# Optimization experiments

Hardware: AMD Instinct MI355X
Metric: run time of the kernel (lower is better)

The kernel has to match this reference:

```python
import jax, jax.numpy as jnp
import numpy as np

N = 50000      # clusters (nodes)
E = 800000     # edges
C_IN = 128     # pt_tr_in_channels
C_OUT = 128    # pt_tr_out_channels
P_HID = 64     # pos_nn hidden
A_HID = 64     # attn_nn hidden
DIM = 2        # pt_tr_dim


def setup_inputs() -> dict:
    key = jax.random.key(0)
    ks = jax.random.split(key, 12)
    def w(k, i, o):
        return jax.random.normal(k, (i, o), jnp.float32) / np.float32(np.sqrt(i))
    return {
        "x": jax.random.normal(ks[0], (N, C_IN), jnp.float32),
        "pos": jax.random.uniform(ks[1], (N, DIM), jnp.float32),
        "edge_index": jax.random.randint(ks[2], (2, E), 0, N),
        # PointTransformerConv linear projections (bias=False in PyG)
        "W_lin": w(ks[3], C_IN, C_OUT),
        "W_src": w(ks[4], C_IN, C_OUT),
        "W_dst": w(ks[5], C_IN, C_OUT),
        # pos_nn MLP [DIM, P_HID, C_OUT], plain_last=False -> ReLU after both layers
        "Wp1": w(ks[6], DIM, P_HID), "bp1": jnp.zeros((P_HID,), jnp.float32),
        "Wp2": w(ks[7], P_HID, C_OUT), "bp2": jnp.zeros((C_OUT,), jnp.float32),
        # attn_nn MLP [C_OUT, A_HID, C_OUT]
        "Wa1": w(ks[8], C_OUT, A_HID), "ba1": jnp.zeros((A_HID,), jnp.float32),
        "Wa2": w(ks[9], A_HID, C_OUT), "ba2": jnp.zeros((C_OUT,), jnp.float32),
    }


def _mlp2(x, W1, b1, W2, b2):
    # PyG MLP(plain_last=False) at eval: Linear -> (identity BN) -> ReLU, twice
    return jax.nn.relu(jax.nn.relu(x @ W1 + b1) @ W2 + b2)


def _segment_softmax(logits, seg, num_segments):
    # per-destination, per-channel stable softmax over incoming edges
    m = jax.ops.segment_max(logits, seg, num_segments=num_segments)  # [N, C]
    e = jnp.exp(logits - m[seg])
    s = jax.ops.segment_sum(e, seg, num_segments=num_segments)
    return e / (s[seg] + 1e-16)


def reference(x, pos, edge_index, W_lin, W_src, W_dst,
              Wp1, bp1, Wp2, bp2, Wa1, ba1, Wa2, ba2):
    src, dst = edge_index[0], edge_index[1]          # message j -> i
    h = x @ W_lin                                     # value path  [N, C]
    a_src = (x @ W_src)[src]                          # alpha_j     [E, C]
    a_dst = (x @ W_dst)[dst]                          # alpha_i     [E, C]
    delta = _mlp2(pos[dst] - pos[src], Wp1, bp1, Wp2, bp2)   # [E, C]
    alpha = _mlp2(a_dst - a_src + delta, Wa1, ba1, Wa2, ba2) # [E, C]
    alpha = _segment_softmax(alpha, dst, N)
    out = jax.ops.segment_sum(alpha * (h[src] + delta), dst, num_segments=N)
    return jax.nn.relu(out)  # out['clusters'].relu()
```

## Files before the change

### kernel.cpp

```cpp
#include <hip/hip_runtime.h>
#include <hip/hip_bf16.h>

#define NN 50000
#define NE 800000

typedef short s16x8 __attribute__((ext_vector_type(8)));
typedef float f32x4 __attribute__((ext_vector_type(4)));

__device__ __forceinline__ unsigned packbf2(float a, float b) {
  __hip_bfloat162 h = __float22bfloat162_rn(make_float2(a, b));
  return *reinterpret_cast<unsigned*>(&h);
}
__device__ __forceinline__ unsigned short bf16rn(float x) {
  return (unsigned short)(packbf2(x, x) & 0xffffu);
}

__global__ __launch_bounds__(256) void zero_counts(int* __restrict__ counts) {
  const int i = blockIdx.x * 256 + threadIdx.x;
  if (i < NN) counts[i] = 0;
}

__global__ __launch_bounds__(256) void count_kernel(const int* __restrict__ ei,
                                                    int* __restrict__ counts) {
  const int e = blockIdx.x * 256 + threadIdx.x;
  if (e < NE) atomicAdd(&counts[ei[NE + e]], 1);
}

__global__ __launch_bounds__(256) void scan_block(const int* __restrict__ counts,
                                                  int* __restrict__ ep,
                                                  int* __restrict__ blocksum) {
  const int i = blockIdx.x * 256 + threadIdx.x;
  const int lane = threadIdx.x & 63;
  const int w = threadIdx.x >> 6;
  const int v = (i < NN) ? counts[i] : 0;
  int s = v;
  #pragma unroll
  for (int off = 1; off < 64; off <<= 1) {
    const int t = __shfl_up(s, off, 64);
    if (lane >= off) s += t;
  }
  __shared__ int wsums[4];
  if (lane == 63) wsums[w] = s;
  __syncthreads();
  int add = 0;
  for (int j = 0; j < w; ++j) add += wsums[j];
  s += add;
  if (i < NN) ep[i] = s - v;
  if (threadIdx.x == 255) blocksum[blockIdx.x] = s;
}

__global__ void scan_tops(const int* __restrict__ blocksum,
                          int* __restrict__ blockoff, int n) {
  const int lane = threadIdx.x;
  int carry = 0;
  for (int base = 0; base < n; base += 64) {
    const int i = base + lane;
    const int v = (i < n) ? blocksum[i] : 0;
    int s = v;
    #pragma unroll
    for (int off = 1; off < 64; off <<= 1) {
      const int t = __shfl_up(s, off, 64);
      if (lane >= off) s += t;
    }
    s += carry;
    if (i < n) blockoff[i] = s - v;
    carry = __shfl(s, 63, 64);
  }
}

__global__ __launch_bounds__(256) void scan_finish(const int* __restrict__ ep,
                                                   const int* __restrict__ blockoff,
                                                   int* __restrict__ cursor,
                                                   int* __restrict__ rowptr) {
  const int i = blockIdx.x * 256 + threadIdx.x;
  if (i < NN) {
    const int v = ep[i] + blockoff[blockIdx.x];
    cursor[i] = v;
    rowptr[i] = v;
  }
  if (i == 0) rowptr[NN] = NE;
}

__global__ __launch_bounds__(256) void scatter_kernel(const int* __restrict__ ei,
                                                      int* __restrict__ cursor,
                                                      int* __restrict__ ssrc,
                                                      int* __restrict__ sdst) {
  const int e = blockIdx.x * 256 + threadIdx.x;
  if (e < NE) {
    const int s = ei[e], d = ei[NE + e];
    const int p = atomicAdd(&cursor[d], 1);
    ssrc[p] = s;
    sdst[p] = d;
  }
}

__global__ __launch_bounds__(256) void fold_w(const float* __restrict__ Wsrc,
                                              const float* __restrict__ Wdst,
                                              const float* __restrict__ Wa1,
                                              float* __restrict__ Wsa,
                                              float* __restrict__ Wda) {
  const int i = blockIdx.x * 256 + threadIdx.x;
  const int m = i >> 13;
  const int kj = i & 8191;
  const int k = kj >> 6, j = kj & 63;
  const float* __restrict__ W = m ? Wdst : Wsrc;
  float acc = 0.f;
  #pragma unroll 4
  for (int q = 0; q < 128; ++q) acc = fmaf(W[k * 128 + q], Wa1[q * 64 + j], acc);
  (m ? Wda : Wsa)[k * 64 + j] = acc;
}

__global__ __launch_bounds__(256) void pack_w(const float* __restrict__ Wp2,
                                              const float* __restrict__ Wa1,
                                              const float* __restrict__ Wa2,
                                              unsigned short* __restrict__ W2B,
                                              unsigned short* __restrict__ Wa1B,
                                              unsigned short* __restrict__ Wa2B) {
  const int t = blockIdx.x * 256 + threadIdx.x;
  if (t >= 24576) return;
  const int u = t & 8191;
  const int j = u & 7, l = (u >> 3) & 63;
  const int lk = (l >> 4) * 8 + j, ln = l & 15;
  if (t < 8192) {
    const int nb = (u >> 9) & 7, kb = u >> 12;
    W2B[u] = bf16rn(Wp2[(kb * 32 + lk) * 128 + nb * 16 + ln]);
  } else if (t < 16384) {
    const int nb = (u >> 9) & 3, kb = u >> 11;
    Wa1B[u] = bf16rn(Wa1[(kb * 32 + lk) * 64 + nb * 16 + ln]);
  } else {
    const int nb = (u >> 9) & 7, kb = u >> 12;
    Wa2B[u] = bf16rn(Wa2[(kb * 32 + lk) * 128 + nb * 16 + ln]);
  }
}

__global__ __launch_bounds__(256) void gemm3_kernel(
    const float* __restrict__ x, const float* __restrict__ Wl,
    const float* __restrict__ Wsa, const float* __restrict__ Wda,
    float* __restrict__ h, float* __restrict__ as1, float* __restrict__ ad1) {
  const int wtask = __builtin_amdgcn_readfirstlane((int)((blockIdx.x * 256 + threadIdx.x) >> 6));
  if (wtask >= 3125 * 4) return;
  const int lane = threadIdx.x & 63;
  const int rg = wtask >> 2;
  const int chunk = wtask & 3;
  const float* __restrict__ W = (chunk <= 1) ? Wl : ((chunk == 2) ? Wsa : Wda);
  float* __restrict__ O = (chunk <= 1) ? h : ((chunk == 2) ? as1 : ad1);
  const int ldw = (chunk <= 1) ? 128 : 64;
  const int col = ((chunk == 1) ? 64 : 0) + lane;
  const int r0 = rg * 16;
  float acc[16];
  #pragma unroll
  for (int r = 0; r < 16; ++r) acc[r] = 0.f;
  const float4* x4 = (const float4*)x;
  #pragma unroll 1
  for (int k4 = 0; k4 < 32; ++k4) {
    const float w0 = W[(size_t)(k4 * 4 + 0) * ldw + col];
    const float w1 = W[(size_t)(k4 * 4 + 1) * ldw + col];
    const float w2 = W[(size_t)(k4 * 4 + 2) * ldw + col];
    const float w3 = W[(size_t)(k4 * 4 + 3) * ldw + col];
    #pragma unroll
    for (int r = 0; r < 16; ++r) {
      const float4 xr = x4[(size_t)(r0 + r) * 32 + k4];
      acc[r] = fmaf(xr.x, w0, fmaf(xr.y, w1, fmaf(xr.z, w2, fmaf(xr.w, w3, acc[r]))));
    }
  }
  #pragma unroll
  for (int r = 0; r < 16; ++r) O[(size_t)(r0 + r) * ldw + col] = acc[r];
}

__global__ __launch_bounds__(256) void edge_mfma(
    const int* __restrict__ ssrc, const int* __restrict__ sdst,
    const int* __restrict__ rowptr, const float* __restrict__ pos,
    const float* __restrict__ hbuf, const float* __restrict__ as1, const float* __restrict__ ad1,
    const float* __restrict__ Wp1, const float* __restrict__ bp1,
    const unsigned short* __restrict__ W2B, const float* __restrict__ bp2,
    const unsigned short* __restrict__ Wa1B, const float* __restrict__ ba1,
    const unsigned short* __restrict__ Wa2B, const float* __restrict__ ba2,
    float* __restrict__ out, float* __restrict__ stag) {
  __shared__ uint4 ldsq[4][384];
  const int wv = threadIdx.x >> 6;
  char* lbase = (char*)&ldsq[wv][0];
  const int lane = threadIdx.x & 63;
  const int g = lane >> 4;
  const int cl = lane & 15;
  const int wid = blockIdx.x * 4 + wv;
  const int wb = wid * 64;

  float cX[8], cY[8];
  #pragma unroll
  for (int nb = 0; nb < 8; ++nb) { cX[nb] = 0.f; cY[nb] = 0.f; }
  int carry_d = -1;

  int myS = ssrc[wb + cl];
  int myD = sdst[wb + cl];
  float2 pD = ((const float2*)pos)[myD];
  float2 pS = ((const float2*)pos)[myS];

  #pragma unroll 1
  for (int st = 0; st < 4; ++st) {
    const int eb = wb + st * 16;
    int myS_n = 0, myD_n = 0;
    if (st < 3) {
      myS_n = ssrc[eb + 16 + cl];
      myD_n = sdst[eb + 16 + cl];
    }
    int dm[4], sm[4];
    #pragma unroll
    for (int i = 0; i < 4; ++i) {
      dm[i] = __shfl(myD, 4 * g + i, 64);
      sm[i] = __shfl(myS, 4 * g + i, 64);
    }
    const int f_d = __shfl(myD, 0, 64);
    const int l_d = __shfl(myD, 15, 64);

    float gDiff[4][4];
    #pragma unroll
    for (int i = 0; i < 4; ++i) {
      #pragma unroll
      for (int nb = 0; nb < 4; ++nb) {
        gDiff[i][nb] = ad1[(size_t)dm[i] * 64 + nb * 16 + cl]
                     - as1[(size_t)sm[i] * 64 + nb * 16 + cl];
      }
    }

    const float p0 = pD.x - pS.x, p1 = pD.y - pS.y;
    s16x8 a1[2];
    #pragma unroll
    for (int kb = 0; kb < 2; ++kb) {
      const int k0 = kb * 32 + g * 8;
      const float4 wA = *(const float4*)(Wp1 + k0);
      const float4 wB = *(const float4*)(Wp1 + k0 + 4);
      const float4 vA = *(const float4*)(Wp1 + 64 + k0);
      const float4 vB = *(const float4*)(Wp1 + 64 + k0 + 4);
      const float4 bA = *(const float4*)(bp1 + k0);
      const float4 bB = *(const float4*)(bp1 + k0 + 4);
      float f0 = fmaxf(fmaf(p0, wA.x, fmaf(p1, vA.x, bA.x)), 0.f);
      float f1 = fmaxf(fmaf(p0, wA.y, fmaf(p1, vA.y, bA.y)), 0.f);
      float f2 = fmaxf(fmaf(p0, wA.z, fmaf(p1, vA.z, bA.z)), 0.f);
      float f3 = fmaxf(fmaf(p0, wA.w, fmaf(p1, vA.w, bA.w)), 0.f);
      float f4 = fmaxf(fmaf(p0, wB.x, fmaf(p1, vB.x, bB.x)), 0.f);
      float f5 = fmaxf(fmaf(p0, wB.y, fmaf(p1, vB.y, bB.y)), 0.f);
      float f6 = fmaxf(fmaf(p0, wB.z, fmaf(p1, vB.z, bB.z)), 0.f);
      float f7 = fmaxf(fmaf(p0, wB.w, fmaf(p1, vB.w, bB.w)), 0.f);
      uint4 q;
      q.x = packbf2(f0, f1); q.y = packbf2(f2, f3);
      q.z = packbf2(f4, f5); q.w = packbf2(f6, f7);
      a1[kb] = __builtin_bit_cast(s16x8, q);
    }

    #pragma unroll
    for (int nb = 0; nb < 8; ++nb) {
      const float bias = bp2[nb * 16 + cl];
      f32x4 acc = {bias, bias, bias, bias};
      const s16x8 b0 = *(const s16x8*)(W2B + ((size_t)(0 * 8 + nb) * 64 + lane) * 8);
      const s16x8 b1 = *(const s16x8*)(W2B + ((size_t)(1 * 8 + nb) * 64 + lane) * 8);
      acc = __builtin_amdgcn_mfma_f32_16x16x32_bf16(a1[0], b0, acc, 0, 0, 0);
      acc = __builtin_amdgcn_mfma_f32_16x16x32_bf16(a1[1], b1, acc, 0, 0, 0);
      #pragma unroll
      for (int i = 0; i < 4; ++i) {
        const int row = g * 4 + i;
        const int byt = (row << 8) + ((((nb * 16 + cl) * 2)) ^ ((row & 7) << 5));
        *(unsigned short*)(lbase + byt) = bf16rn(fmaxf(acc[i], 0.f));
      }
    }

    float2 pD_n = pD, pS_n = pS;
    if (st < 3) {
      pD_n = ((const float2*)pos)[myD_n];
      pS_n = ((const float2*)pos)[myS_n];
    }

    s16x8 a2[4];
    #pragma unroll
    for (int kb = 0; kb < 4; ++kb) {
      const int byt = (cl << 8) + ((kb * 64 + g * 16) ^ ((cl & 7) << 5));
      a2[kb] = __builtin_bit_cast(s16x8, *(const uint4*)(lbase + byt));
    }

    #pragma unroll
    for (int nb = 0; nb < 4; ++nb) {
      const float b1v = ba1[nb * 16 + cl];
      f32x4 acc = {gDiff[0][nb] + b1v, gDiff[1][nb] + b1v,
                   gDiff[2][nb] + b1v, gDiff[3][nb] + b1v};
      #pragma unroll
      for (int kb = 0; kb < 4; ++kb) {
        const s16x8 b = *(const s16x8*)(Wa1B + ((size_t)(kb * 4 + nb) * 64 + lane) * 8);
        acc = __builtin_amdgcn_mfma_f32_16x16x32_bf16(a2[kb], b, acc, 0, 0, 0);
      }
      #pragma unroll
      for (int i = 0; i < 4; ++i) {
        const int row = g * 4 + i;
        const int byt = 4096 + (row << 7) + ((((nb * 16 + cl) * 2)) ^ ((row & 7) << 4));
        *(unsigned short*)(lbase + byt) = bf16rn(fmaxf(acc[i], 0.f));
      }
    }
    s16x8 a3[2];
    #pragma unroll
    for (int kb = 0; kb < 2; ++kb) {
      const int byt = 4096 + (cl << 7) + ((kb * 64 + g * 16) ^ ((cl & 7) << 4));
      a3[kb] = __builtin_bit_cast(s16x8, *(const uint4*)(lbase + byt));
    }

    const bool eq01 = dm[0] == dm[1], eq12 = dm[1] == dm[2], eq23 = dm[2] == dm[3];
    bool r_[4];
    r_[3] = true; r_[2] = eq23; r_[1] = eq12 && eq23; r_[0] = eq01 && eq12 && eq23;
    const int dnx = __shfl(myD, (4 * g + 4) & 15, 64);
    const bool cont = (g < 3) && (dm[3] == dnx);
    const float fullf = r_[0] ? 1.f : 0.f;
    const float fulln = __shfl_down(fullf, 16, 64);
    const int dpv = __shfl(myD, (4 * g - 1) & 15, 64);
    bool head[4];
    head[0] = (g == 0) ? true : (dm[0] != dpv);
    head[1] = dm[1] != dm[0];
    head[2] = dm[2] != dm[1];
    head[3] = dm[3] != dm[2];
    bool fin[4];
    #pragma unroll
    for (int i = 0; i < 4; ++i)
      fin[i] = head[i] && !(g == 0 && i == 0) && (dm[i] != l_d);

    const bool mismatch = (st != 0) && (carry_d != f_d);
    const bool seed = (st == 0) || mismatch;
    const bool closeFirst = (f_d != l_d);
    const int oldd = carry_d;
    int fo_final = 0, fo_slot = 0;
    if (mismatch) {
      const int q0 = rowptr[oldd], q1 = rowptr[oldd + 1];
      if (q0 >= wb && q1 <= wb + 64) fo_final = 1;
      else fo_slot = 2 * wid + ((q0 < wb) ? 0 : 1);
    }
    int fc_final = 0, fc_slot = 0;
    if (closeFirst) {
      const int q0 = rowptr[f_d], q1 = rowptr[f_d + 1];
      if (q0 >= wb && q1 <= wb + 64) fc_final = 1;
      else fc_slot = 2 * wid + ((q0 < wb) ? 0 : 1);
    }
    const unsigned long long bal = __ballot(myD == l_d);
    const int m_h = (int)__builtin_ctzll(bal & 0xffffull);
    const int i_h = m_h & 3, g_h = m_h >> 2;

    float hgn[4];
    #pragma unroll
    for (int i = 0; i < 4; ++i) hgn[i] = hbuf[(size_t)sm[i] * 128 + cl];
    #pragma unroll
    for (int nb = 0; nb < 8; ++nb) {
      float del[4];
      #pragma unroll
      for (int i = 0; i < 4; ++i) {
        const int row = g * 4 + i;
        const int byt = (row << 8) + ((((nb * 16 + cl) * 2)) ^ ((row & 7) << 5));
        const unsigned short uu = *(const unsigned short*)(lbase + byt);
        del[i] = __builtin_bit_cast(float, ((unsigned)uu) << 16);
      }
      float hgc[4];
      #pragma unroll
      for (int i = 0; i < 4; ++i) hgc[i] = hgn[i];
      if (nb < 7) {
        #pragma unroll
        for (int i = 0; i < 4; ++i)
          hgn[i] = hbuf[(size_t)sm[i] * 128 + (nb + 1) * 16 + cl];
      }
      const float b2v = ba2[nb * 16 + cl];
      f32x4 acc3 = {b2v, b2v, b2v, b2v};
      {
        const s16x8 b0 = *(const s16x8*)(Wa2B + ((size_t)(0 * 8 + nb) * 64 + lane) * 8);
        const s16x8 b1 = *(const s16x8*)(Wa2B + ((size_t)(1 * 8 + nb) * 64 + lane) * 8);
        acc3 = __builtin_amdgcn_mfma_f32_16x16x32_bf16(a3[0], b0, acc3, 0, 0, 0);
        acc3 = __builtin_amdgcn_mfma_f32_16x16x32_bf16(a3[1], b1, acc3, 0, 0, 0);
      }
      float x[4], y[4];
      #pragma unroll
      for (int i = 0; i < 4; ++i) {
        const float ee = __expf(fmaxf(acc3[i], 0.f));
        y[i] = ee;
        x[i] = ee * (hgc[i] + del[i]);
      }
      const float sx3 = x[3],                      sy3 = y[3];
      const float sx2 = x[2] + (eq23 ? sx3 : 0.f), sy2 = y[2] + (eq23 ? sy3 : 0.f);
      const float sx1 = x[1] + (eq12 ? sx2 : 0.f), sy1 = y[1] + (eq12 ? sy2 : 0.f);
      const float sx0 = x[0] + (eq01 ? sx1 : 0.f), sy0 = y[0] + (eq01 ? sy1 : 0.f);
      float Bx = 0.f, By = 0.f;
      #pragma unroll
      for (int tt = 0; tt < 3; ++tt) {
        const float nsx = __shfl_down(sx0, 16, 64);
        const float nsy = __shfl_down(sy0, 16, 64);
        const float nBx = __shfl_down(Bx, 16, 64);
        const float nBy = __shfl_down(By, 16, 64);
        Bx = cont ? (nsx + (fulln > 0.5f ? nBx : 0.f)) : 0.f;
        By = cont ? (nsy + (fulln > 0.5f ? nBy : 0.f)) : 0.f;
      }
      float hx[4], hy[4];
      #pragma unroll
      for (int i = 0; i < 4; ++i) {
        hx[i] = ((i == 0) ? sx0 : (i == 1) ? sx1 : (i == 2) ? sx2 : sx3) + (r_[i] ? Bx : 0.f);
        hy[i] = ((i == 0) ? sy0 : (i == 1) ? sy1 : (i == 2) ? sy2 : sy3) + (r_[i] ? By : 0.f);
      }
      const float h0x = __shfl(hx[0], cl, 64);
      const float h0y = __shfl(hy[0], cl, 64);
      if (mismatch && g == 0) {
        if (fo_final) {
          out[(size_t)oldd * 128 + nb * 16 + cl] = fmaxf(cX[nb] / (cY[nb] + 1e-16f), 0.f);
        } else {
          stag[(size_t)fo_slot * 256 + nb * 16 + cl] = cY[nb];
          stag[(size_t)fo_slot * 256 + 128 + nb * 16 + cl] = cX[nb];
        }
      }
      if (seed) { cX[nb] = h0x; cY[nb] = h0y; }
      else      { cX[nb] += h0x; cY[nb] += h0y; }
      if (closeFirst) {
        if (g == 0) {
          if (fc_final) {
            out[(size_t)f_d * 128 + nb * 16 + cl] = fmaxf(cX[nb] / (cY[nb] + 1e-16f), 0.f);
          } else {
            stag[(size_t)fc_slot * 256 + nb * 16 + cl] = cY[nb];
            stag[(size_t)fc_slot * 256 + 128 + nb * 16 + cl] = cX[nb];
          }
        }
        #pragma unroll
        for (int i = 0; i < 4; ++i)
          if (fin[i])
            out[(size_t)dm[i] * 128 + nb * 16 + cl] = fmaxf(hx[i] / (hy[i] + 1e-16f), 0.f);
        const float selx = (i_h == 0) ? hx[0] : (i_h == 1) ? hx[1] : (i_h == 2) ? hx[2] : hx[3];
        const float sely = (i_h == 0) ? hy[0] : (i_h == 1) ? hy[1] : (i_h == 2) ? hy[2] : hy[3];
        cX[nb] = __shfl(selx, g_h * 16 + cl, 64);
        cY[nb] = __shfl(sely, g_h * 16 + cl, 64);
      }
    }
    carry_d = l_d;
    myS = myS_n; myD = myD_n; pD = pD_n; pS = pS_n;
  }

  {
    const int q0 = rowptr[carry_d], q1 = rowptr[carry_d + 1];
    const bool ffin = (q0 >= wb) && (q1 <= wb + 64);
    const int fslot = 2 * wid + ((q0 < wb) ? 0 : 1);
    if (g == 0) {
      #pragma unroll
      for (int nb = 0; nb < 8; ++nb) {
        if (ffin) {
          out[(size_t)carry_d * 128 + nb * 16 + cl] = fmaxf(cX[nb] / (cY[nb] + 1e-16f), 0.f);
        } else {
          stag[(size_t)fslot * 256 + nb * 16 + cl] = cY[nb];
          stag[(size_t)fslot * 256 + 128 + nb * 16 + cl] = cX[nb];
        }
      }
    }
  }
}

__global__ __launch_bounds__(256) void finalize_kernel(const int* __restrict__ rowptr,
                                                       const float* __restrict__ stag,
                                                       float* __restrict__ out) {
  const int idx = blockIdx.x * 256 + threadIdx.x;
  const int d = idx >> 5;
  const int c4 = idx & 31;
  if (d >= NN) return;
  const int r0 = rowptr[d];
  const int r1 = rowptr[d + 1];
  float4* o4 = (float4*)(out + (size_t)d * 128 + c4 * 4);
  if (r0 == r1) {
    const float4 z = {0.f, 0.f, 0.f, 0.f};
    *o4 = z;
    return;
  }
  const int w0 = r0 >> 6;
  const int w1 = (r1 - 1) >> 6;
  if (w0 == w1) return;
  float ee0 = 0.f, ee1 = 0.f, ee2 = 0.f, ee3 = 0.f;
  float vv0 = 0.f, vv1 = 0.f, vv2 = 0.f, vv3 = 0.f;
  int slot = 2 * w0 + 1;
  for (int w = w0; w <= w1; ++w) {
    const float* sp = stag + (size_t)slot * 256;
    const float4 a = *(const float4*)(sp + c4 * 4);
    const float4 b = *(const float4*)(sp + 128 + c4 * 4);
    ee0 += a.x; ee1 += a.y; ee2 += a.z; ee3 += a.w;
    vv0 += b.x; vv1 += b.y; vv2 += b.z; vv3 += b.w;
    slot = 2 * (w + 1);
  }
  float4 r;
  r.x = fmaxf(vv0 / (ee0 + 1e-16f), 0.f);
  r.y = fmaxf(vv1 / (ee1 + 1e-16f), 0.f);
  r.z = fmaxf(vv2 / (ee2 + 1e-16f), 0.f);
  r.w = fmaxf(vv3 / (ee3 + 1e-16f), 0.f);
  *o4 = r;
}

extern "C" void kernel_launch(void* const* d_in, const int* in_sizes, int n_in,
                              void* d_out, int out_size, void* d_ws, size_t ws_size,
                              hipStream_t stream) {
  const float* x     = (const float*)d_in[0];
  const float* pos   = (const float*)d_in[1];
  const int*   ei    = (const int*)d_in[2];
  const float* W_lin = (const float*)d_in[3];
  const float* W_src = (const float*)d_in[4];
  const float* W_dst = (const float*)d_in[5];
  const float* Wp1   = (const float*)d_in[6];
  const float* bp1   = (const float*)d_in[7];
  const float* Wp2   = (const float*)d_in[8];
  const float* bp2   = (const float*)d_in[9];
  const float* Wa1   = (const float*)d_in[10];
  const float* ba1   = (const float*)d_in[11];
  const float* Wa2   = (const float*)d_in[12];
  const float* ba2   = (const float*)d_in[13];
  float* out = (float*)d_out;

  float* h    = (float*)d_ws;
  float* as1  = h   + (size_t)NN * 128;
  float* ad1  = as1 + (size_t)NN * 64;
  float* stag = ad1 + (size_t)NN * 64;
  float* Wsa  = stag + (size_t)25000 * 256;
  float* Wda  = Wsa + 128 * 64;
  unsigned short* W2B  = (unsigned short*)(Wda + 128 * 64);
  unsigned short* Wa1B = W2B + 8192;
  unsigned short* Wa2B = Wa1B + 8192;
  int* counts   = (int*)(Wa2B + 8192);
  int* ep       = counts + NN;
  int* cursor   = ep + NN;
  int* rowptr   = cursor + NN;
  int* blocksum = rowptr + NN + 1;
  int* blockoff = blocksum + 196;
  int* ssrc     = blockoff + 196;
  int* sdst     = ssrc + NE;

  zero_counts<<<196, 256, 0, stream>>>(counts);
  count_kernel<<<3125, 256, 0, stream>>>(ei, counts);
  scan_block<<<196, 256, 0, stream>>>(counts, ep, blocksum);
  scan_tops<<<1, 64, 0, stream>>>(blocksum, blockoff, 196);
  scan_finish<<<196, 256, 0, stream>>>(ep, blockoff, cursor, rowptr);
  scatter_kernel<<<3125, 256, 0, stream>>>(ei, cursor, ssrc, sdst);
  fold_w<<<64, 256, 0, stream>>>(W_src, W_dst, Wa1, Wsa, Wda);
  pack_w<<<96, 256, 0, stream>>>(Wp2, Wa1, Wa2, W2B, Wa1B, Wa2B);
  gemm3_kernel<<<3125, 256, 0, stream>>>(x, W_lin, Wsa, Wda, h, as1, ad1);
  edge_mfma<<<3125, 256, 0, stream>>>(ssrc, sdst, rowptr, pos, h, as1, ad1,
                                      Wp1, bp1, W2B, bp2, Wa1B, ba1, Wa2B, ba2,
                                      out, stag);
  finalize_kernel<<<6250, 256, 0, stream>>>(rowptr, stag, out);
}
```

Baseline: 576.9 us.

## Split each 64-edge tile across two waves by output-channel halves

Each 64-edge tile is now handled by a pair of waves that share one LDS staging buffer. Each wave computes half the output channels of the pos MLP, attention hidden layer and final accumulation, and block-level barriers coordinate the shared LDS writes and reads. The grid doubles to keep the same edge coverage, and per-wave register use (accumulators, gathers) drops, which can raise occupancy and parallelism. In exchange, both waves redo the index shuffles, position MLP input and segment bookkeeping, and the added __syncthreads calls couple the waves in a block.

```diff
diff --git a/kernel.cpp b/kernel.cpp
--- a/kernel.cpp
+++ b/kernel.cpp
@@ -176,18 +176,22 @@
     const unsigned short* __restrict__ Wa1B, const float* __restrict__ ba1,
     const unsigned short* __restrict__ Wa2B, const float* __restrict__ ba2,
     float* __restrict__ out, float* __restrict__ stag) {
-  __shared__ uint4 ldsq[4][384];
+  __shared__ uint4 ldsq[2][384];
   const int wv = threadIdx.x >> 6;
-  char* lbase = (char*)&ldsq[wv][0];
+  const int g2 = wv >> 1;
+  const int half = wv & 1;
+  char* lbase = (char*)&ldsq[g2][0];
   const int lane = threadIdx.x & 63;
   const int g = lane >> 4;
   const int cl = lane & 15;
-  const int wid = blockIdx.x * 4 + wv;
+  const int wid = blockIdx.x * 2 + g2;
   const int wb = wid * 64;
-
-  float cX[8], cY[8];
+  const int nbB8 = half * 4;
+  const int nbB4 = half * 2;
+
+  float cX[4], cY[4];
   #pragma unroll
-  for (int nb = 0; nb < 8; ++nb) { cX[nb] = 0.f; cY[nb] = 0.f; }
+  for (int n = 0; n < 4; ++n) { cX[n] = 0.f; cY[n] = 0.f; }
   int carry_d = -1;
 
   int myS = ssrc[wb + cl];
@@ -212,13 +216,13 @@
     const int f_d = __shfl(myD, 0, 64);
     const int l_d = __shfl(myD, 15, 64);
 
-    float gDiff[4][4];
+    float gDiff[4][2];
     #pragma unroll
     for (int i = 0; i < 4; ++i) {
       #pragma unroll
-      for (int nb = 0; nb < 4; ++nb) {
-        gDiff[i][nb] = ad1[(size_t)dm[i] * 64 + nb * 16 + cl]
-                     - as1[(size_t)sm[i] * 64 + nb * 16 + cl];
+      for (int n = 0; n < 2; ++n) {
+        const int col = (nbB4 + n) * 16 + cl;
+        gDiff[i][n] = ad1[(size_t)dm[i] * 64 + col] - as1[(size_t)sm[i] * 64 + col];
       }
     }
 
@@ -248,7 +252,8 @@
     }
 
     #pragma unroll
-    for (int nb = 0; nb < 8; ++nb) {
+    for (int n = 0; n < 4; ++n) {
+      const int nb = nbB8 + n;
       const float bias = bp2[nb * 16 + cl];
       f32x4 acc = {bias, bias, bias, bias};
       const s16x8 b0 = *(const s16x8*)(W2B + ((size_t)(0 * 8 + nb) * 64 + lane) * 8);
@@ -269,6 +274,8 @@
       pS_n = ((const float2*)pos)[myS_n];
     }
 
+    __syncthreads();
+
     s16x8 a2[4];
     #pragma unroll
     for (int kb = 0; kb < 4; ++kb) {
@@ -277,10 +284,11 @@
     }
 
     #pragma unroll
-    for (int nb = 0; nb < 4; ++nb) {
+    for (int n = 0; n < 2; ++n) {
+      const int nb = nbB4 + n;
       const float b1v = ba1[nb * 16 + cl];
-      f32x4 acc = {gDiff[0][nb] + b1v, gDiff[1][nb] + b1v,
-                   gDiff[2][nb] + b1v, gDiff[3][nb] + b1v};
+      f32x4 acc = {gDiff[0][n] + b1v, gDiff[1][n] + b1v,
+                   gDiff[2][n] + b1v, gDiff[3][n] + b1v};
       #pragma unroll
       for (int kb = 0; kb < 4; ++kb) {
         const s16x8 b = *(const s16x8*)(Wa1B + ((size_t)(kb * 4 + nb) * 64 + lane) * 8);
@@ -293,6 +301,9 @@
         *(unsigned short*)(lbase + byt) = bf16rn(fmaxf(acc[i], 0.f));
       }
     }
+
+    __syncthreads();
+
     s16x8 a3[2];
     #pragma unroll
     for (int kb = 0; kb < 2; ++kb) {
@@ -340,9 +351,10 @@
 
     float hgn[4];
     #pragma unroll
-    for (int i = 0; i < 4; ++i) hgn[i] = hbuf[(size_t)sm[i] * 128 + cl];
-    #pragma unroll
-    for (int nb = 0; nb < 8; ++nb) {
+    for (int i = 0; i < 4; ++i) hgn[i] = hbuf[(size_t)sm[i] * 128 + nbB8 * 16 + cl];
+    #pragma unroll
+    for (int n = 0; n < 4; ++n) {
+      const int nb = nbB8 + n;
       float del[4];
       #pragma unroll
       for (int i = 0; i < 4; ++i) {
@@ -354,7 +366,7 @@
       float hgc[4];
       #pragma unroll
       for (int i = 0; i < 4; ++i) hgc[i] = hgn[i];
-      if (nb < 7) {
+      if (n < 3) {
         #pragma unroll
         for (int i = 0; i < 4; ++i)
           hgn[i] = hbuf[(size_t)sm[i] * 128 + (nb + 1) * 16 + cl];
@@ -398,21 +410,21 @@
       const float h0y = __shfl(hy[0], cl, 64);
       if (mismatch && g == 0) {
         if (fo_final) {
-          out[(size_t)oldd * 128 + nb * 16 + cl] = fmaxf(cX[nb] / (cY[nb] + 1e-16f), 0.f);
+          out[(size_t)oldd * 128 + nb * 16 + cl] = fmaxf(cX[n] / (cY[n] + 1e-16f), 0.f);
         } else {
-          stag[(size_t)fo_slot * 256 + nb * 16 + cl] = cY[nb];
-          stag[(size_t)fo_slot * 256 + 128 + nb * 16 + cl] = cX[nb];
+          stag[(size_t)fo_slot * 256 + nb * 16 + cl] = cY[n];
+          stag[(size_t)fo_slot * 256 + 128 + nb * 16 + cl] = cX[n];
         }
       }
-      if (seed) { cX[nb] = h0x; cY[nb] = h0y; }
-      else      { cX[nb] += h0x; cY[nb] += h0y; }
+      if (seed) { cX[n] = h0x; cY[n] = h0y; }
+      else      { cX[n] += h0x; cY[n] += h0y; }
       if (closeFirst) {
         if (g == 0) {
           if (fc_final) {
-            out[(size_t)f_d * 128 + nb * 16 + cl] = fmaxf(cX[nb] / (cY[nb] + 1e-16f), 0.f);
+            out[(size_t)f_d * 128 + nb * 16 + cl] = fmaxf(cX[n] / (cY[n] + 1e-16f), 0.f);
           } else {
-            stag[(size_t)fc_slot * 256 + nb * 16 + cl] = cY[nb];
-            stag[(size_t)fc_slot * 256 + 128 + nb * 16 + cl] = cX[nb];
+            stag[(size_t)fc_slot * 256 + nb * 16 + cl] = cY[n];
+            stag[(size_t)fc_slot * 256 + 128 + nb * 16 + cl] = cX[n];
           }
         }
         #pragma unroll
@@ -421,8 +433,8 @@
             out[(size_t)dm[i] * 128 + nb * 16 + cl] = fmaxf(hx[i] / (hy[i] + 1e-16f), 0.f);
         const float selx = (i_h == 0) ? hx[0] : (i_h == 1) ? hx[1] : (i_h == 2) ? hx[2] : hx[3];
         const float sely = (i_h == 0) ? hy[0] : (i_h == 1) ? hy[1] : (i_h == 2) ? hy[2] : hy[3];
-        cX[nb] = __shfl(selx, g_h * 16 + cl, 64);
-        cY[nb] = __shfl(sely, g_h * 16 + cl, 64);
+        cX[n] = __shfl(selx, g_h * 16 + cl, 64);
+        cY[n] = __shfl(sely, g_h * 16 + cl, 64);
       }
     }
     carry_d = l_d;
@@ -435,12 +447,13 @@
     const int fslot = 2 * wid + ((q0 < wb) ? 0 : 1);
     if (g == 0) {
       #pragma unroll
-      for (int nb = 0; nb < 8; ++nb) {
+      for (int n = 0; n < 4; ++n) {
+        const int nb = nbB8 + n;
         if (ffin) {
-          out[(size_t)carry_d * 128 + nb * 16 + cl] = fmaxf(cX[nb] / (cY[nb] + 1e-16f), 0.f);
+          out[(size_t)carry_d * 128 + nb * 16 + cl] = fmaxf(cX[n] / (cY[n] + 1e-16f), 0.f);
         } else {
-          stag[(size_t)fslot * 256 + nb * 16 + cl] = cY[nb];
-          stag[(size_t)fslot * 256 + 128 + nb * 16 + cl] = cX[nb];
+          stag[(size_t)fslot * 256 + nb * 16 + cl] = cY[n];
+          stag[(size_t)fslot * 256 + 128 + nb * 16 + cl] = cX[n];
         }
       }
     }
@@ -530,7 +543,7 @@
   fold_w<<<64, 256, 0, stream>>>(W_src, W_dst, Wa1, Wsa, Wda);
   pack_w<<<96, 256, 0, stream>>>(Wp2, Wa1, Wa2, W2B, Wa1B, Wa2B);
   gemm3_kernel<<<3125, 256, 0, stream>>>(x, W_lin, Wsa, Wda, h, as1, ad1);
-  edge_mfma<<<3125, 256, 0, stream>>>(ssrc, sdst, rowptr, pos, h, as1, ad1,
+  edge_mfma<<<6250, 256, 0, stream>>>(ssrc, sdst, rowptr, pos, h, as1, ad1,
                                       Wp1, bp1, W2B, bp2, Wa1B, ba1, Wa2B, ba2,
                                       out, stag);
   finalize_kernel<<<6250, 256, 0, stream>>>(rowptr, stag, out);
```

Result: slower. 657.9 us (+14.0%).
